# Performance work log

Measured on AMD Instinct MI355X. Metric: run time of the kernel, lower is better.

Reference implementation:

```python
import jax, jax.numpy as jnp
import numpy as np

N, D = 65536, 256


def _unit(x):
    # contrastive embeddings are L2-normalized; also keeps exp(dot) finite
    return x / jnp.linalg.norm(x, axis=-1, keepdims=True)


def setup_inputs() -> dict:
    key = jax.random.key(0)
    k1, k2 = jax.random.split(key)
    z_a = _unit(jax.random.normal(k1, (N, D), dtype=jnp.float32))
    z_b = _unit(jax.random.normal(k2, (N, D), dtype=jnp.float32))
    return {"z_a": z_a, "z_b": z_b}


def reference(z_a, z_b):
    # d_i = dot(z_a[i], z_b[i])  (the only quantity the original ever computes)
    n = z_a.shape[0]
    d = jnp.sum(z_a * z_b, axis=-1)  # [n]
    # Original loop structure:
    #   alignment      = sum_i (-d_i)
    #   negative_sum_i = (# of j in range(n-1), j != i) * d_i
    #                  = (n-2) * d_i for i < n-1, (n-1) * d_i for i == n-1
    #   uniformity_i   = exp(d_i)
    counts = jnp.full((n,), n - 2, dtype=d.dtype).at[n - 1].set(n - 1)
    return jnp.sum((counts - 1.0) * d + jnp.exp(d))
```

## Files before the change

kernel.cpp:

```cpp
#include <hip/hip_runtime.h>
#include <math.h>


#define D_DIM 256
#define ROWS_PER_WAVE 32
#define WAVES_PER_BLOCK 4

__global__ __launch_bounds__(256, 2)
void dot_loss_partial(const float4* __restrict__ za4,
                      const float4* __restrict__ zb4,
                      float* __restrict__ partial,
                      int n) {
    const int lane = threadIdx.x & 63;
    const int wave = threadIdx.x >> 6;
    const int waveId = blockIdx.x * WAVES_PER_BLOCK + wave;
    const int row0 = waveId * ROWS_PER_WAVE;

    __shared__ float part[WAVES_PER_BLOCK][ROWS_PER_WAVE][65];

    const float4* a = za4 + (size_t)row0 * 64 + lane;
    const float4* b = zb4 + (size_t)row0 * 64 + lane;

    #pragma unroll 8
    for (int r = 0; r < ROWS_PER_WAVE; ++r) {
        float4 av = a[(size_t)r * 64];
        float4 bv = b[(size_t)r * 64];
        float t = av.x * bv.x;
        t = fmaf(av.y, bv.y, t);
        t = fmaf(av.z, bv.z, t);
        t = fmaf(av.w, bv.w, t);
        part[wave][r][lane] = t;
    }
    __builtin_amdgcn_s_waitcnt(0);

    const int rowIdx = lane & 31;
    const int colBase = (lane >> 5) * 32;
    float s = 0.0f;
    #pragma unroll
    for (int c = 0; c < 32; ++c)
        s += part[wave][rowIdx][colBase + c];

    float d = s + __shfl_down(s, 32);

    float acc = 0.0f;
    if (lane < 32) {
        int row = row0 + rowIdx;
        float coeff = (row == n - 1) ? (float)(n - 2) : (float)(n - 3);
        acc = coeff * d + expf(d);
    }

    #pragma unroll
    for (int off = 16; off > 0; off >>= 1)
        acc += __shfl_down(acc, off);

    __shared__ float smem[WAVES_PER_BLOCK];
    if (lane == 0) smem[wave] = acc;
    __syncthreads();
    if (threadIdx.x == 0) {
        float s2 = 0.0f;
        #pragma unroll
        for (int w = 0; w < WAVES_PER_BLOCK; ++w) s2 += smem[w];
        partial[blockIdx.x] = s2;
    }
}

__global__ __launch_bounds__(256)
void reduce_partials(const float* __restrict__ partial,
                     float* __restrict__ out,
                     int m) {
    const int lane = threadIdx.x & 63;
    const int wave = threadIdx.x >> 6;
    double s = 0.0;
    for (int i = threadIdx.x; i < m; i += 256)
        s += (double)partial[i];
    #pragma unroll
    for (int off = 32; off > 0; off >>= 1)
        s += __shfl_down(s, off);
    __shared__ double smem[4];
    if (lane == 0) smem[wave] = s;
    __syncthreads();
    if (threadIdx.x == 0)
        out[0] = (float)(smem[0] + smem[1] + smem[2] + smem[3]);
}

extern "C" void kernel_launch(void* const* d_in, const int* in_sizes, int n_in,
                              void* d_out, int out_size, void* d_ws, size_t ws_size,
                              hipStream_t stream) {
    const float4* za4 = (const float4*)d_in[0];
    const float4* zb4 = (const float4*)d_in[1];
    float* out = (float*)d_out;
    float* partial = (float*)d_ws;
    const int n = in_sizes[0] / D_DIM;
    const int blocks = n / (ROWS_PER_WAVE * WAVES_PER_BLOCK);

    dot_loss_partial<<<blocks, 256, 0, stream>>>(za4, zb4, partial, n);
    reduce_partials<<<1, 256, 0, stream>>>(partial, out, blocks);
}
```

Baseline: 142.8 us.

## Load rows directly into LDS via global_load_lds and cut rows per wave

Replaces register loads plus a per-lane partial-sum LDS transpose with direct global-to-LDS async loads (global_load_lds, 16 bytes per lane), then each lane computes a slice of the row dot product from LDS using a rotated access pattern to avoid bank conflicts. Rows per wave drop from 32 to 8, so the grid has four times as many blocks and each holds a small 64 KB LDS staging buffer. The aim is to issue memory traffic without register staging and to get more waves in flight. The risk is that the larger LDS footprint limits occupancy and adds an extra LDS read pass.

```diff
diff --git a/kernel.cpp b/kernel.cpp
--- a/kernel.cpp
+++ b/kernel.cpp
@@ -3,55 +3,67 @@
 
 
 #define D_DIM 256
-#define ROWS_PER_WAVE 32
+#define ROWS_PER_WAVE 8
 #define WAVES_PER_BLOCK 4
+
+typedef __attribute__((address_space(1))) const unsigned int gu32_t;
+typedef __attribute__((address_space(3))) unsigned int su32_t;
+
+__device__ __forceinline__ void gload_lds16(const void* g, void* l) {
+    __builtin_amdgcn_global_load_lds((gu32_t*)g, (su32_t*)l, 16, 0, 0);
+}
 
 __global__ __launch_bounds__(256, 2)
 void dot_loss_partial(const float4* __restrict__ za4,
                       const float4* __restrict__ zb4,
                       float* __restrict__ partial,
                       int n) {
+    __shared__ __align__(16) float A[WAVES_PER_BLOCK][ROWS_PER_WAVE][D_DIM];
+    __shared__ __align__(16) float B[WAVES_PER_BLOCK][ROWS_PER_WAVE][D_DIM];
+
     const int lane = threadIdx.x & 63;
     const int wave = threadIdx.x >> 6;
-    const int waveId = blockIdx.x * WAVES_PER_BLOCK + wave;
-    const int row0 = waveId * ROWS_PER_WAVE;
-
-    __shared__ float part[WAVES_PER_BLOCK][ROWS_PER_WAVE][65];
+    const int row0 = (blockIdx.x * WAVES_PER_BLOCK + wave) * ROWS_PER_WAVE;
 
     const float4* a = za4 + (size_t)row0 * 64 + lane;
     const float4* b = zb4 + (size_t)row0 * 64 + lane;
 
-    #pragma unroll 8
+    #pragma unroll
     for (int r = 0; r < ROWS_PER_WAVE; ++r) {
-        float4 av = a[(size_t)r * 64];
-        float4 bv = b[(size_t)r * 64];
-        float t = av.x * bv.x;
-        t = fmaf(av.y, bv.y, t);
-        t = fmaf(av.z, bv.z, t);
-        t = fmaf(av.w, bv.w, t);
-        part[wave][r][lane] = t;
+        gload_lds16(a + (size_t)r * 64, &A[wave][r][0]);
+        gload_lds16(b + (size_t)r * 64, &B[wave][r][0]);
     }
     __builtin_amdgcn_s_waitcnt(0);
+    __builtin_amdgcn_sched_barrier(0);
 
-    const int rowIdx = lane & 31;
-    const int colBase = (lane >> 5) * 32;
+    const int rowIdx = lane & 7;
+    const int cj = lane >> 3;
+    const float4* Ar = reinterpret_cast<const float4*>(&A[wave][rowIdx][0]);
+    const float4* Br = reinterpret_cast<const float4*>(&B[wave][rowIdx][0]);
     float s = 0.0f;
     #pragma unroll
-    for (int c = 0; c < 32; ++c)
-        s += part[wave][rowIdx][colBase + c];
-
-    float d = s + __shfl_down(s, 32);
+    for (int c = 0; c < 8; ++c) {
+        const int f = cj * 8 + ((c + rowIdx) & 7);
+        float4 av = Ar[f];
+        float4 bv = Br[f];
+        s = fmaf(av.x, bv.x, s);
+        s = fmaf(av.y, bv.y, s);
+        s = fmaf(av.z, bv.z, s);
+        s = fmaf(av.w, bv.w, s);
+    }
+    s += __shfl_down(s, 32);
+    s += __shfl_down(s, 16);
+    s += __shfl_down(s, 8);
 
     float acc = 0.0f;
-    if (lane < 32) {
-        int row = row0 + rowIdx;
-        float coeff = (row == n - 1) ? (float)(n - 2) : (float)(n - 3);
-        acc = coeff * d + expf(d);
+    if (lane < 8) {
+        const int row = row0 + lane;
+        const float coeff = (row == n - 1) ? (float)(n - 2) : (float)(n - 3);
+        acc = coeff * s + expf(s);
     }
-
-    #pragma unroll
-    for (int off = 16; off > 0; off >>= 1)
-        acc += __shfl_down(acc, off);
+    acc += __shfl_down(acc, 4);
+    acc += __shfl_down(acc, 2);
+    acc += __shfl_down(acc, 1);
 
     __shared__ float smem[WAVES_PER_BLOCK];
     if (lane == 0) smem[wave] = acc;
```

New measurement: 145.4 us. No clear change (+1.9%).
